# Kernel optimization log

Hardware: AMD Instinct MI355X
Metric: run time of the kernel (lower is better)

The kernel has to match this reference:

```python
import jax, jax.numpy as jnp
import numpy as np

BATCH = 32      # init batch_size
HID = 256       # init hidden_dim
SENT = 64       # sentence_size
WORDS = 64      # words per sentence (the -1 in the view)
N = BATCH * SENT


def setup_inputs() -> dict:
    key = jax.random.key(0)
    k1, k2, k3, k4 = jax.random.split(key, 4)
    stdv_lin = 1.0 / np.sqrt(HID)
    x = jax.random.normal(k1, (N, WORDS, HID), dtype=jnp.float32)
    W = jax.random.uniform(k2, (HID, HID), jnp.float32, -stdv_lin, stdv_lin)
    b = jax.random.uniform(k3, (HID,), jnp.float32, -stdv_lin, stdv_lin)
    context = jax.random.uniform(k4, (HID,), jnp.float32, -stdv_lin, stdv_lin)
    return {"x": x, "W": W, "b": b, "context": context, "sentence_size": SENT}


def reference(x, W, b, context, sentence_size):
    # tanh(Linear(x)) applied per position; vectorized over the batch loop
    attends = jnp.tanh(jnp.einsum("nwh,oh->nwo", x, W) + b)  # [N, WORDS, HID]
    scores = attends * context                                 # [N, WORDS, HID]
    # nn.Softmax on the [-1, HID] view -> softmax over the hidden dim
    alpha = jax.nn.softmax(scores, axis=-1)                    # [N, WORDS, HID]
    attended = x * alpha                                       # legacy same-numel mul
    attended = attended.reshape(BATCH, sentence_size, -1, HID)
    return jnp.sum(attended, axis=2)                           # [BATCH, SENT, HID]
```

## Files before the change

kernel.cpp:

```cpp
#include <hip/hip_runtime.h>
#include <hip/hip_bf16.h>

#define HID 256
#define NROWS 2048
#define NITER 8
#define GRID (NROWS / NITER)
#define PITCH 264
#define TILE_F (64 * 256)

typedef __attribute__((ext_vector_type(8))) short short8;
typedef __attribute__((ext_vector_type(4))) float float4v;
typedef __attribute__((ext_vector_type(4))) unsigned int uint4v;

__device__ __forceinline__ float bf2f(unsigned short u) {
    return __uint_as_float(((unsigned int)u) << 16);
}

__device__ __forceinline__ unsigned int pk_bf16(float a, float b) {
    __hip_bfloat162 p = __float22bfloat162_rn(float2{a, b});
    return *(unsigned int*)&p;
}

__device__ __forceinline__ void bar_sync() {
    __builtin_amdgcn_sched_barrier(0);
    asm volatile("s_waitcnt lgkmcnt(0)");
    __builtin_amdgcn_s_barrier();
    __builtin_amdgcn_sched_barrier(0);
}

__device__ __forceinline__ float row16_sum(float v) {
    float t;
    t = __builtin_bit_cast(float, __builtin_amdgcn_update_dpp(
            0, __builtin_bit_cast(int, v), 0xB1, 0xf, 0xf, true));
    v += t;
    t = __builtin_bit_cast(float, __builtin_amdgcn_update_dpp(
            0, __builtin_bit_cast(int, v), 0x4E, 0xf, 0xf, true));
    v += t;
    t = __builtin_bit_cast(float, __builtin_amdgcn_update_dpp(
            0, __builtin_bit_cast(int, v), 0x124, 0xf, 0xf, true));
    v += t;
    t = __builtin_bit_cast(float, __builtin_amdgcn_update_dpp(
            0, __builtin_bit_cast(int, v), 0x128, 0xf, 0xf, true));
    v += t;
    return v;
}

__global__ __launch_bounds__(512, 2) void attend_fused(
    const float* __restrict__ x, const float* __restrict__ W,
    const float* __restrict__ bias, const float* __restrict__ ctx,
    float* __restrict__ out)
{
    __shared__ unsigned short xs[2][64 * PITCH];
    __shared__ float wsum[8][64];
    __shared__ float rinv[64];

    const int tid  = threadIdx.x;
    const int wave = tid >> 6;
    const int lane = tid & 63;
    const int q    = lane >> 4;
    const int c    = lane & 15;
    const int obase = wave * 32;
    const int n0 = blockIdx.x * NITER;

    float4v R[8];
    {
        const float4v* xv = (const float4v*)(x + (size_t)n0 * TILE_F);
#pragma unroll
        for (int i = 0; i < 8; ++i) R[i] = xv[tid + 512 * i];
    }

    float bb[2], m2[2], ec[2];
    short8 bfrag[8][2];
#pragma unroll
    for (int nt = 0; nt < 2; ++nt) {
        const int o = obase + 2 * c + nt;
        bb[nt] = bias[o];
        const float cv = ctx[o];
        m2[nt] = cv * -2.8853900817779268f;
        ec[nt] = __builtin_amdgcn_exp2f(cv * 1.4426950408889634f);
        const float* wr = W + (size_t)o * 256 + q * 8;
#pragma unroll
        for (int kt = 0; kt < 8; ++kt) {
            float4v w0 = *(const float4v*)(wr + kt * 32);
            float4v w1 = *(const float4v*)(wr + kt * 32 + 4);
            uint4v u = { pk_bf16(w0.x, w0.y), pk_bf16(w0.z, w0.w),
                         pk_bf16(w1.x, w1.y), pk_bf16(w1.z, w1.w) };
            bfrag[kt][nt] = __builtin_bit_cast(short8, u);
        }
    }

#pragma unroll
    for (int i = 0; i < 8; ++i) {
        const int chunk = tid + 512 * i;
        const int r = chunk >> 6, col4 = (chunk & 63) * 4;
        uint2 u;
        u.x = pk_bf16(R[i].x, R[i].y);
        u.y = pk_bf16(R[i].z, R[i].w);
        *(uint2*)&xs[0][r * PITCH + col4] = u;
    }
    {
        const float4v* xv = (const float4v*)(x + (size_t)(n0 + 1) * TILE_F);
#pragma unroll
        for (int i = 0; i < 8; ++i) R[i] = xv[tid + 512 * i];
    }
    bar_sync();

    int cur = 0;
#pragma unroll 1
    for (int it = 0; it < NITER; ++it) {
        const unsigned short* xsc = xs[cur];

        float4v acc[4][2];
#pragma unroll
        for (int mt = 0; mt < 4; ++mt)
#pragma unroll
            for (int nt = 0; nt < 2; ++nt)
                acc[mt][nt] = (float4v){0.f, 0.f, 0.f, 0.f};

#pragma unroll
        for (int kt = 0; kt < 8; ++kt) {
            short8 a[4];
#pragma unroll
            for (int mt = 0; mt < 4; ++mt)
                a[mt] = *(const short8*)&xsc[(mt * 16 + c) * PITCH + kt * 32 + q * 8];
#pragma unroll
            for (int nt = 0; nt < 2; ++nt)
#pragma unroll
                for (int mt = 0; mt < 4; ++mt)
                    acc[mt][nt] = __builtin_amdgcn_mfma_f32_16x16x32_bf16(
                        a[mt], bfrag[kt][nt], acc[mt][nt], 0, 0, 0);
        }

        float psum[4][4];
#pragma unroll
        for (int mt = 0; mt < 4; ++mt)
#pragma unroll
            for (int r = 0; r < 4; ++r)
                psum[mt][r] = 0.f;

#pragma unroll
        for (int nt = 0; nt < 2; ++nt) {
#pragma unroll
            for (int mt = 0; mt < 4; ++mt) {
#pragma unroll
                for (int r = 0; r < 4; ++r) {
                    const float y  = acc[mt][nt][r] + bb[nt];
                    const float E  = __builtin_amdgcn_exp2f(y * 2.8853900817779268f);
                    const float rd = __builtin_amdgcn_rcpf(E + 1.0f);
                    const float e  = ec[nt] * __builtin_amdgcn_exp2f(m2[nt] * rd);
                    acc[mt][nt][r] = e;
                    psum[mt][r] += e;
                }
            }
        }
#pragma unroll
        for (int mt = 0; mt < 4; ++mt)
#pragma unroll
            for (int r = 0; r < 4; ++r)
                psum[mt][r] = row16_sum(psum[mt][r]);
        if (c == 0) {
#pragma unroll
            for (int mt = 0; mt < 4; ++mt) {
                float4v p = {psum[mt][0], psum[mt][1], psum[mt][2], psum[mt][3]};
                *(float4v*)&wsum[wave][mt * 16 + q * 4] = p;
            }
        }
        bar_sync();
        if (tid < 64) {
            const float t = wsum[0][tid] + wsum[1][tid] + wsum[2][tid] + wsum[3][tid]
                          + wsum[4][tid] + wsum[5][tid] + wsum[6][tid] + wsum[7][tid];
            rinv[tid] = __builtin_amdgcn_rcpf(t);
        }
        bar_sync();

        float ri[4][4];
#pragma unroll
        for (int mt = 0; mt < 4; ++mt)
#pragma unroll
            for (int r = 0; r < 4; ++r)
                ri[mt][r] = rinv[mt * 16 + q * 4 + r];

        float outp[2] = {0.f, 0.f};
#pragma unroll
        for (int mt = 0; mt < 4; ++mt) {
#pragma unroll
            for (int r = 0; r < 4; ++r) {
                const int w = mt * 16 + q * 4 + r;
                unsigned int pair = *(const unsigned int*)&xsc[w * PITCH + obase + 2 * c];
                const float wgt = ri[mt][r];
                outp[0] += bf2f((unsigned short)pair)         * (acc[mt][0][r] * wgt);
                outp[1] += bf2f((unsigned short)(pair >> 16)) * (acc[mt][1][r] * wgt);
            }
        }
#pragma unroll
        for (int nt = 0; nt < 2; ++nt) {
            float v = outp[nt];
            v += __shfl_xor(v, 16);
            v += __shfl_xor(v, 32);
            outp[nt] = v;
        }
        if (q == 0)
            *(float2*)&out[(size_t)(n0 + it) * HID + obase + 2 * c] = float2{outp[0], outp[1]};

        if (it + 1 < NITER) {
            unsigned short* xsn = (unsigned short*)xs[cur ^ 1];
#pragma unroll
            for (int i = 0; i < 8; ++i) {
                const int chunk = tid + 512 * i;
                const int r = chunk >> 6, col4 = (chunk & 63) * 4;
                uint2 u;
                u.x = pk_bf16(R[i].x, R[i].y);
                u.y = pk_bf16(R[i].z, R[i].w);
                *(uint2*)&xsn[r * PITCH + col4] = u;
            }
            if (it + 2 < NITER) {
                const float4v* xv = (const float4v*)(x + (size_t)(n0 + it + 2) * TILE_F);
#pragma unroll
                for (int i = 0; i < 8; ++i) R[i] = xv[tid + 512 * i];
            }
        }
        bar_sync();
        cur ^= 1;
    }
}

extern "C" void kernel_launch(void* const* d_in, const int* in_sizes, int n_in,
                              void* d_out, int out_size, void* d_ws, size_t ws_size,
                              hipStream_t stream) {
    const float* x    = (const float*)d_in[0];
    const float* W    = (const float*)d_in[1];
    const float* bias = (const float*)d_in[2];
    const float* ctx  = (const float*)d_in[3];
    (void)in_sizes; (void)n_in; (void)d_ws; (void)ws_size;

    attend_fused<<<GRID, 512, 0, stream>>>(x, W, bias, ctx, (float*)d_out);
}
```

Measured before the change: 207.4 us.

## Split sentence tiles into half-tiles to double grid and raise occupancy

Each block now processes 4 sentences as 8 half-tiles of 32 words instead of 8 full 64-word tiles. This halves LDS and register footprint, raises launch bounds to 4 blocks per CU, and doubles the grid so each CU gets more resident waves to hide global-load latency. The weighted output sum is now accumulated across two half-tiles before it is stored. The tanh/exp epilogue is also rewritten as exp2(ctx*log2e*(1-2/(E+1))), which drops one multiply. The cost is twice as many barrier rounds per unit of work, and the W fragment and bias setup is repeated across twice as many blocks.

```diff
diff --git a/kernel.cpp b/kernel.cpp
--- a/kernel.cpp
+++ b/kernel.cpp
@@ -3,10 +3,11 @@
 
 #define HID 256
 #define NROWS 2048
-#define NITER 8
-#define GRID (NROWS / NITER)
+#define NPB 4
+#define NHT (NPB * 2)
+#define GRID (NROWS / NPB)
 #define PITCH 264
-#define TILE_F (64 * 256)
+#define HTF (32 * 256)
 
 typedef __attribute__((ext_vector_type(8))) short short8;
 typedef __attribute__((ext_vector_type(4))) float float4v;
@@ -45,14 +46,14 @@
     return v;
 }
 
-__global__ __launch_bounds__(512, 2) void attend_fused(
+__global__ __launch_bounds__(512, 4) void attend_fused(
     const float* __restrict__ x, const float* __restrict__ W,
     const float* __restrict__ bias, const float* __restrict__ ctx,
     float* __restrict__ out)
 {
-    __shared__ unsigned short xs[2][64 * PITCH];
-    __shared__ float wsum[8][64];
-    __shared__ float rinv[64];
+    __shared__ unsigned short xs[2][32 * PITCH];
+    __shared__ float wsum[8][32];
+    __shared__ float rinv[32];
 
     const int tid  = threadIdx.x;
     const int wave = tid >> 6;
@@ -60,24 +61,22 @@
     const int q    = lane >> 4;
     const int c    = lane & 15;
     const int obase = wave * 32;
-    const int n0 = blockIdx.x * NITER;
-
-    float4v R[8];
+    const float* xp = x + (size_t)blockIdx.x * (NPB * 64 * 256);
+
+    float4v R[4];
     {
-        const float4v* xv = (const float4v*)(x + (size_t)n0 * TILE_F);
-#pragma unroll
-        for (int i = 0; i < 8; ++i) R[i] = xv[tid + 512 * i];
-    }
-
-    float bb[2], m2[2], ec[2];
+        const float4v* xv = (const float4v*)xp;
+#pragma unroll
+        for (int j = 0; j < 4; ++j) R[j] = xv[tid + 512 * j];
+    }
+
+    float bb[2], f2[2];
     short8 bfrag[8][2];
 #pragma unroll
     for (int nt = 0; nt < 2; ++nt) {
         const int o = obase + 2 * c + nt;
         bb[nt] = bias[o];
-        const float cv = ctx[o];
-        m2[nt] = cv * -2.8853900817779268f;
-        ec[nt] = __builtin_amdgcn_exp2f(cv * 1.4426950408889634f);
+        f2[nt] = ctx[o] * 1.4426950408889634f;
         const float* wr = W + (size_t)o * 256 + q * 8;
 #pragma unroll
         for (int kt = 0; kt < 8; ++kt) {
@@ -90,50 +89,51 @@
     }
 
 #pragma unroll
-    for (int i = 0; i < 8; ++i) {
-        const int chunk = tid + 512 * i;
+    for (int j = 0; j < 4; ++j) {
+        const int chunk = tid + 512 * j;
         const int r = chunk >> 6, col4 = (chunk & 63) * 4;
         uint2 u;
-        u.x = pk_bf16(R[i].x, R[i].y);
-        u.y = pk_bf16(R[i].z, R[i].w);
+        u.x = pk_bf16(R[j].x, R[j].y);
+        u.y = pk_bf16(R[j].z, R[j].w);
         *(uint2*)&xs[0][r * PITCH + col4] = u;
     }
     {
-        const float4v* xv = (const float4v*)(x + (size_t)(n0 + 1) * TILE_F);
-#pragma unroll
-        for (int i = 0; i < 8; ++i) R[i] = xv[tid + 512 * i];
+        const float4v* xv = (const float4v*)(xp + HTF);
+#pragma unroll
+        for (int j = 0; j < 4; ++j) R[j] = xv[tid + 512 * j];
     }
     bar_sync();
 
+    float oacc[2] = {0.f, 0.f};
     int cur = 0;
 #pragma unroll 1
-    for (int it = 0; it < NITER; ++it) {
+    for (int h = 0; h < NHT; ++h) {
         const unsigned short* xsc = xs[cur];
 
-        float4v acc[4][2];
-#pragma unroll
-        for (int mt = 0; mt < 4; ++mt)
+        float4v acc[2][2];
+#pragma unroll
+        for (int mt = 0; mt < 2; ++mt)
 #pragma unroll
             for (int nt = 0; nt < 2; ++nt)
                 acc[mt][nt] = (float4v){0.f, 0.f, 0.f, 0.f};
 
 #pragma unroll
         for (int kt = 0; kt < 8; ++kt) {
-            short8 a[4];
-#pragma unroll
-            for (int mt = 0; mt < 4; ++mt)
+            short8 a[2];
+#pragma unroll
+            for (int mt = 0; mt < 2; ++mt)
                 a[mt] = *(const short8*)&xsc[(mt * 16 + c) * PITCH + kt * 32 + q * 8];
 #pragma unroll
             for (int nt = 0; nt < 2; ++nt)
 #pragma unroll
-                for (int mt = 0; mt < 4; ++mt)
+                for (int mt = 0; mt < 2; ++mt)
                     acc[mt][nt] = __builtin_amdgcn_mfma_f32_16x16x32_bf16(
                         a[mt], bfrag[kt][nt], acc[mt][nt], 0, 0, 0);
         }
 
-        float psum[4][4];
-#pragma unroll
-        for (int mt = 0; mt < 4; ++mt)
+        float psum[2][4];
+#pragma unroll
+        for (int mt = 0; mt < 2; ++mt)
 #pragma unroll
             for (int r = 0; r < 4; ++r)
                 psum[mt][r] = 0.f;
@@ -141,82 +141,86 @@
 #pragma unroll
         for (int nt = 0; nt < 2; ++nt) {
 #pragma unroll
-            for (int mt = 0; mt < 4; ++mt) {
+            for (int mt = 0; mt < 2; ++mt) {
 #pragma unroll
                 for (int r = 0; r < 4; ++r) {
                     const float y  = acc[mt][nt][r] + bb[nt];
                     const float E  = __builtin_amdgcn_exp2f(y * 2.8853900817779268f);
                     const float rd = __builtin_amdgcn_rcpf(E + 1.0f);
-                    const float e  = ec[nt] * __builtin_amdgcn_exp2f(m2[nt] * rd);
+                    const float t  = __builtin_fmaf(-2.0f, rd, 1.0f);
+                    const float e  = __builtin_amdgcn_exp2f(f2[nt] * t);
                     acc[mt][nt][r] = e;
                     psum[mt][r] += e;
                 }
             }
         }
 #pragma unroll
-        for (int mt = 0; mt < 4; ++mt)
+        for (int mt = 0; mt < 2; ++mt)
 #pragma unroll
             for (int r = 0; r < 4; ++r)
                 psum[mt][r] = row16_sum(psum[mt][r]);
         if (c == 0) {
 #pragma unroll
-            for (int mt = 0; mt < 4; ++mt) {
+            for (int mt = 0; mt < 2; ++mt) {
                 float4v p = {psum[mt][0], psum[mt][1], psum[mt][2], psum[mt][3]};
                 *(float4v*)&wsum[wave][mt * 16 + q * 4] = p;
             }
         }
         bar_sync();
-        if (tid < 64) {
+        if (tid < 32) {
             const float t = wsum[0][tid] + wsum[1][tid] + wsum[2][tid] + wsum[3][tid]
                           + wsum[4][tid] + wsum[5][tid] + wsum[6][tid] + wsum[7][tid];
             rinv[tid] = __builtin_amdgcn_rcpf(t);
         }
         bar_sync();
 
-        float ri[4][4];
-#pragma unroll
-        for (int mt = 0; mt < 4; ++mt)
+        float ri[2][4];
+#pragma unroll
+        for (int mt = 0; mt < 2; ++mt)
 #pragma unroll
             for (int r = 0; r < 4; ++r)
                 ri[mt][r] = rinv[mt * 16 + q * 4 + r];
 
-        float outp[2] = {0.f, 0.f};
-#pragma unroll
-        for (int mt = 0; mt < 4; ++mt) {
+#pragma unroll
+        for (int mt = 0; mt < 2; ++mt) {
 #pragma unroll
             for (int r = 0; r < 4; ++r) {
                 const int w = mt * 16 + q * 4 + r;
                 unsigned int pair = *(const unsigned int*)&xsc[w * PITCH + obase + 2 * c];
                 const float wgt = ri[mt][r];
-                outp[0] += bf2f((unsigned short)pair)         * (acc[mt][0][r] * wgt);
-                outp[1] += bf2f((unsigned short)(pair >> 16)) * (acc[mt][1][r] * wgt);
-            }
-        }
-#pragma unroll
-        for (int nt = 0; nt < 2; ++nt) {
-            float v = outp[nt];
-            v += __shfl_xor(v, 16);
-            v += __shfl_xor(v, 32);
-            outp[nt] = v;
-        }
-        if (q == 0)
-            *(float2*)&out[(size_t)(n0 + it) * HID + obase + 2 * c] = float2{outp[0], outp[1]};
-
-        if (it + 1 < NITER) {
-            unsigned short* xsn = (unsigned short*)xs[cur ^ 1];
-#pragma unroll
-            for (int i = 0; i < 8; ++i) {
-                const int chunk = tid + 512 * i;
+                oacc[0] += bf2f((unsigned short)pair)         * (acc[mt][0][r] * wgt);
+                oacc[1] += bf2f((unsigned short)(pair >> 16)) * (acc[mt][1][r] * wgt);
+            }
+        }
+        if (h & 1) {
+#pragma unroll
+            for (int nt = 0; nt < 2; ++nt) {
+                float v = oacc[nt];
+                v += __shfl_xor(v, 16);
+                v += __shfl_xor(v, 32);
+                oacc[nt] = v;
+            }
+            if (q == 0) {
+                const size_t n = (size_t)blockIdx.x * NPB + (h >> 1);
+                *(float2*)&out[n * HID + obase + 2 * c] = float2{oacc[0], oacc[1]};
+            }
+            oacc[0] = 0.f; oacc[1] = 0.f;
+        }
+
+        if (h + 1 < NHT) {
+#pragma unroll
+            for (int j = 0; j < 4; ++j) {
+                const int chunk = tid + 512 * j;
                 const int r = chunk >> 6, col4 = (chunk & 63) * 4;
                 uint2 u;
-                u.x = pk_bf16(R[i].x, R[i].y);
-                u.y = pk_bf16(R[i].z, R[i].w);
-                *(uint2*)&xsn[r * PITCH + col4] = u;
-            }
-            if (it + 2 < NITER) {
-                const float4v* xv = (const float4v*)(x + (size_t)(n0 + it + 2) * TILE_F);
-#pragma unroll
-                for (int i = 0; i < 8; ++i) R[i] = xv[tid + 512 * i];
+                u.x = pk_bf16(R[j].x, R[j].y);
+                u.y = pk_bf16(R[j].z, R[j].w);
+                *(uint2*)&xs[cur ^ 1][r * PITCH + col4] = u;
+            }
+            if (h + 2 < NHT) {
+                const float4v* xv = (const float4v*)(xp + (size_t)(h + 2) * HTF);
+#pragma unroll
+                for (int j = 0; j < 4; ++j) R[j] = xv[tid + 512 * j];
             }
         }
         bar_sync();
```

Measured after the change: 213.5 us. 1.03x slower.
